# Performance work log

Measured on AMD Instinct MI355X. Metric: run time of the kernel, lower is better.

## Reference

```python
import jax, jax.numpy as jnp
import numpy as np

IN_FEATURES = 1024
OUT_FEATURES = 1024
KNOT_COUNT = 5
ORDER = 3
BATCH = 4096


def setup_inputs() -> dict:
    key = jax.random.key(0)
    k1, k2 = jax.random.split(key)
    x = jax.random.normal(k1, (BATCH, IN_FEATURES), dtype=jnp.float32)
    knots = jnp.linspace(-1.0, 1.0, KNOT_COUNT, dtype=jnp.float32)
    coeffs = jax.random.normal(k2, (KNOT_COUNT + ORDER, OUT_FEATURES, IN_FEATURES), dtype=jnp.float32)
    return {"x": x, "knots": knots, "coeffs": coeffs}


def _bspline_bases(x, knots, order):
    # x: [B, I]; knots: [K] uniform grid. Extend to K + 2*order + 1 knots so
    # the number of degree-`order` basis functions is K + order.
    h = knots[1] - knots[0]
    left = knots[0] + h * jnp.arange(-order, 0, dtype=knots.dtype)
    right = knots[-1] + h * jnp.arange(1, order + 2, dtype=knots.dtype)
    t = jnp.concatenate([left, knots, right])  # [K + 2*order + 1]
    xe = x[..., None]  # [B, I, 1]
    # degree-0 indicator bases: [B, I, m-1]
    bases = ((xe >= t[:-1]) & (xe < t[1:])).astype(x.dtype)
    # Cox-de Boor recursion up to degree `order` (vectorized over batch/features)
    for k in range(1, order + 1):
        left_num = (xe - t[: -(k + 1)]) / (t[k:-1] - t[: -(k + 1)])
        right_num = (t[k + 1:] - xe) / (t[k + 1:] - t[1:-k])
        bases = left_num * bases[..., :-1] + right_num * bases[..., 1:]
    return bases  # [B, I, K + order]


def reference(x, knots, coeffs):
    # Faithful fused version of the per-(i,j) python loops:
    # spline_j(b) = sum_n B_n(x[b,i]) * coeffs[n, j, i]; output sums over i.
    bases = _bspline_bases(x, knots, ORDER)          # [B, I, N]
    return jnp.einsum('bin,noi->bo', bases, coeffs)  # [B, O]
```

## Files before the change

### kernel.cpp

```cpp
#include <hip/hip_runtime.h>
#include <hip/hip_bf16.h>
#include <cstdint>
#include <cstddef>

#define IN_F   1024
#define OUT_F  1024
#define NB     8
#define BATCH  4096
#define KTOT   (NB * IN_F)

typedef __attribute__((ext_vector_type(4))) float  f32x4;
typedef __attribute__((ext_vector_type(8))) float  f32x8;
typedef __attribute__((ext_vector_type(8))) __bf16 bf16x8;
typedef __attribute__((ext_vector_type(4))) unsigned short u16x4;

#define GLDS16(g, l)                                                     \
    __builtin_amdgcn_global_load_lds(                                    \
        (const __attribute__((address_space(1))) void*)(g),              \
        (__attribute__((address_space(3))) void*)(l), 16, 0, 0)

__device__ __forceinline__ void spline_w(float r, float w[4]) {
    const float r2 = r * r, r3 = r2 * r;
    const float omr = 1.0f - r;
    w[0] = omr * omr * omr * (1.0f / 6.0f);
    w[1] = (3.0f * r3 - 6.0f * r2 + 4.0f) * (1.0f / 6.0f);
    w[2] = (-3.0f * r3 + 3.0f * r2 + 3.0f * r + 1.0f) * (1.0f / 6.0f);
    w[3] = r3 * (1.0f / 6.0f);
}

__global__ void k_cvt(const float* __restrict__ src, __bf16* __restrict__ dst) {
    const size_t g   = blockIdx.x * blockDim.x + threadIdx.x;
    const size_t idx = g * 8;
    const int i = (int)(idx & 1023);
    const int o = (int)((idx >> 10) & 1023);
    const int c = (i >> 3) & 7;
    const int isw = (i & ~63) | ((c ^ (o & 7)) << 3);
    f32x8 v = *(const f32x8*)(src + idx);
    bf16x8 ov = __builtin_convertvector(v, bf16x8);
    *(bf16x8*)(dst + (idx - i) + isw) = ov;
}

__global__ void k_basis(const float* __restrict__ x, __bf16* __restrict__ A) {
    const int g    = blockIdx.x * blockDim.x + threadIdx.x;
    const int flat = g * 4;
    const int b = flat >> 10, i = flat & 1023;
    f32x4 xv = *(const f32x4*)(x + flat);

    float w[4][4];
    int   jj[4];
#pragma unroll
    for (int e = 0; e < 4; ++e) {
        const float u  = (xv[e] + 2.5f) * 2.0f;
        const float jf = floorf(u);
        jj[e] = (int)jf;
        spline_w(u - jf, w[e]);
    }

    const int c   = (i >> 3) & 7;
    const int isw = (i & ~63) | ((c ^ (b & 7)) << 3) | (i & 7);
    __bf16* base = A + (size_t)b * KTOT + isw;
#pragma unroll
    for (int n = 0; n < NB; ++n) {
        u16x4 pack;
#pragma unroll
        for (int e = 0; e < 4; ++e) {
            const int d = n - jj[e] + 3;
            float v = (d == 0) ? w[e][0]
                    : (d == 1) ? w[e][1]
                    : (d == 2) ? w[e][2]
                    : (d == 3) ? w[e][3] : 0.0f;
            __bf16 h = (__bf16)v;
            pack[e] = __builtin_bit_cast(unsigned short, h);
        }
        *(u16x4*)(base + n * IN_F) = pack;
    }
}

#define BM 128
#define BN 128
#define BK 64
#define NT (KTOT / BK)
#define SPLITK 2
#define NTS (NT / SPLITK)

__global__ __launch_bounds__(512) void k_gemm(const __bf16* __restrict__ A,
                                              const __bf16* __restrict__ W,
                                              float* __restrict__ C,
                                              float* __restrict__ P) {
    __shared__ __align__(16) char ls[2][32768];

    const int tid  = threadIdx.x;
    const int o0   = blockIdx.x * BN;
    const int b0   = blockIdx.y * BM;
    const int kz   = blockIdx.z;
    const int lane = tid & 63;
    const int wv   = tid >> 6;
    const int wr   = wv >> 2;
    const int wc   = wv & 3;
    const int l15  = lane & 15;
    const int lhi  = lane >> 4;

    f32x4 acc[4][2] = {};

    const int srow  = tid >> 3;
    const int scol8 = (tid & 7) * 8;

    auto STAGE = [&](int buf, int kt) {
        const int k0 = kt * BK;
        const int n  = k0 >> 10;
        const int i0 = k0 & 1023;
        char* la = ls[buf];
        char* lb = ls[buf] + 16384;
#pragma unroll
        for (int it = 0; it < 2; ++it) {
            const __bf16* ga = A + (size_t)(b0 + srow + it * 64) * KTOT + k0 + scol8;
            GLDS16(ga, la + tid * 16 + it * 8192);
        }
#pragma unroll
        for (int it = 0; it < 2; ++it) {
            const __bf16* gw = W + ((size_t)n << 20)
                                 + (size_t)(o0 + srow + it * 64) * IN_F + i0 + scol8;
            GLDS16(gw, lb + tid * 16 + it * 8192);
        }
    };

    const int ktBeg = kz * NTS;
    STAGE(0, ktBeg);
    __syncthreads();

    int cur = 0;
    for (int kt = ktBeg; kt < ktBeg + NTS; ++kt) {
        if (kt + 1 < ktBeg + NTS) STAGE(cur ^ 1, kt + 1);
        const char* la = ls[cur];
        const char* lb = ls[cur] + 16384;
#pragma unroll
        for (int kk = 0; kk < BK; kk += 32) {
            bf16x8 af[4], bfr[2];
#pragma unroll
            for (int m = 0; m < 4; ++m) {
                const int r = wr * 64 + m * 16 + l15;
                const int c = ((kk >> 3) + lhi) ^ (r & 7);
                af[m] = *(const bf16x8*)(la + r * 128 + c * 16);
            }
#pragma unroll
            for (int nn = 0; nn < 2; ++nn) {
                const int r = wc * 32 + nn * 16 + l15;
                const int c = ((kk >> 3) + lhi) ^ (r & 7);
                bfr[nn] = *(const bf16x8*)(lb + r * 128 + c * 16);
            }
#pragma unroll
            for (int m = 0; m < 4; ++m)
#pragma unroll
                for (int nn = 0; nn < 2; ++nn)
                    acc[m][nn] = __builtin_amdgcn_mfma_f32_16x16x32_bf16(
                        af[m], bfr[nn], acc[m][nn], 0, 0, 0);
        }
        __syncthreads();
        cur ^= 1;
    }

    float* dst = (kz == 0) ? C : P;
    const int crow = lhi * 4;
#pragma unroll
    for (int m = 0; m < 4; ++m) {
#pragma unroll
        for (int nn = 0; nn < 2; ++nn) {
            float* cp = dst + (size_t)(b0 + wr * 64 + m * 16 + crow) * OUT_F
                            + o0 + wc * 32 + nn * 16 + l15;
#pragma unroll
            for (int j = 0; j < 4; ++j)
                cp[(size_t)j * OUT_F] = acc[m][nn][j];
        }
    }
}

__global__ void k_add(float* __restrict__ C, const float* __restrict__ P) {
    const size_t g = (size_t)(blockIdx.x * blockDim.x + threadIdx.x) * 4;
    f32x4 a = *(const f32x4*)(C + g);
    f32x4 b = *(const f32x4*)(P + g);
    a += b;
    *(f32x4*)(C + g) = a;
}

__global__ void k_naive(const float* __restrict__ x, const float* __restrict__ coeffs,
                        float* __restrict__ out) {
    const int b = blockIdx.y * 16 + (threadIdx.x >> 4);
    const int o = blockIdx.x * 16 + (threadIdx.x & 15);
    float sum = 0.0f;
    for (int i = 0; i < IN_F; ++i) {
        const float u  = (x[(size_t)b * IN_F + i] + 2.5f) * 2.0f;
        const float jf = floorf(u);
        const int   j  = (int)jf;
        float w[4];
        spline_w(u - jf, w);
#pragma unroll
        for (int m = 0; m < 4; ++m) {
            const int idx = j - 3 + m;
            if (idx >= 0 && idx < NB)
                sum += w[m] * coeffs[(size_t)idx * OUT_F * IN_F + (size_t)o * IN_F + i];
        }
    }
    out[(size_t)b * OUT_F + o] = sum;
}

extern "C" void kernel_launch(void* const* d_in, const int* in_sizes, int n_in,
                              void* d_out, int out_size, void* d_ws, size_t ws_size,
                              hipStream_t stream) {
    const float* x      = (const float*)d_in[0];
    const float* coeffs = (const float*)d_in[2];
    float* out = (float*)d_out;

    const size_t needA = (size_t)BATCH * KTOT * sizeof(__bf16);
    const size_t needW = (size_t)NB * OUT_F * IN_F * sizeof(__bf16);
    const size_t needP = (size_t)BATCH * OUT_F * sizeof(float);

    if (ws_size >= needA + needW + needP) {
        __bf16* A  = (__bf16*)d_ws;
        __bf16* Wb = (__bf16*)((char*)d_ws + needA);
        float*  P  = (float*)((char*)d_ws + needA + needW);

        hipLaunchKernelGGL(k_cvt, dim3(NB * OUT_F * IN_F / 8 / 256), dim3(256), 0,
                           stream, coeffs, Wb);
        hipLaunchKernelGGL(k_basis, dim3(BATCH * IN_F / 4 / 256), dim3(256), 0,
                           stream, x, A);
        hipLaunchKernelGGL(k_gemm, dim3(OUT_F / BN, BATCH / BM, SPLITK), dim3(512),
                           0, stream, A, Wb, out, P);
        hipLaunchKernelGGL(k_add, dim3(BATCH * OUT_F / 4 / 256), dim3(256), 0,
                           stream, out, P);
    } else if (ws_size >= needA + needW) {
        __bf16* A  = (__bf16*)d_ws;
        __bf16* Wb = (__bf16*)((char*)d_ws + needA);
        hipLaunchKernelGGL(k_cvt, dim3(NB * OUT_F * IN_F / 8 / 256), dim3(256), 0,
                           stream, coeffs, Wb);
        hipLaunchKernelGGL(k_basis, dim3(BATCH * IN_F / 4 / 256), dim3(256), 0,
                           stream, x, A);
        hipLaunchKernelGGL(k_naive, dim3(OUT_F / 16, BATCH / 16), dim3(256), 0,
                           stream, x, coeffs, out);
    } else {
        hipLaunchKernelGGL(k_naive, dim3(OUT_F / 16, BATCH / 16), dim3(256), 0,
                           stream, x, coeffs, out);
    }
}
```

Baseline: 132.8 us.

## Enlarge GEMM tile to 256x128, triple-buffer LDS, and remap blocks across XCDs

The bf16 GEMM tile grows from 128x128 to 256x128, so each wave now computes a 64x64 sub-tile. This gives more MFMA work per LDS fragment load and raises arithmetic intensity. Double buffering becomes a three-stage LDS pipeline that uses explicit vmcnt waits and raw barriers, so global-to-LDS loads run further ahead of compute. A flat 256-block grid is remapped so neighbouring batch tiles land on the same XCD for L2 reuse. The costs are 144KB of LDS, which limits occupancy to one block per CU, a higher accumulator register count, and dropping an unused fallback path.

```diff
diff --git a/kernel.cpp b/kernel.cpp
--- a/kernel.cpp
+++ b/kernel.cpp
@@ -76,31 +76,38 @@
     }
 }
 
-#define BM 128
+#define BM 256
 #define BN 128
 #define BK 64
 #define NT (KTOT / BK)
 #define SPLITK 2
 #define NTS (NT / SPLITK)
+#define BUFSZ 49152
 
 __global__ __launch_bounds__(512) void k_gemm(const __bf16* __restrict__ A,
                                               const __bf16* __restrict__ W,
                                               float* __restrict__ C,
                                               float* __restrict__ P) {
-    __shared__ __align__(16) char ls[2][32768];
-
+    __shared__ __align__(16) char ls[3 * BUFSZ];
+
+    const int fid = blockIdx.x;
+    const int xcd = fid & 7;
+    const int s   = fid >> 3;
+    const int y   = xcd + 8 * (s & 1);
+    const int xb  = (s >> 1) & 7;
+    const int kz  = s >> 4;
+
+    const int o0   = xb * BN;
+    const int b0   = y * BM;
     const int tid  = threadIdx.x;
-    const int o0   = blockIdx.x * BN;
-    const int b0   = blockIdx.y * BM;
-    const int kz   = blockIdx.z;
     const int lane = tid & 63;
     const int wv   = tid >> 6;
-    const int wr   = wv >> 2;
-    const int wc   = wv & 3;
+    const int wr   = wv >> 1;
+    const int wc   = wv & 1;
     const int l15  = lane & 15;
     const int lhi  = lane >> 4;
 
-    f32x4 acc[4][2] = {};
+    f32x4 acc[4][4] = {};
 
     const int srow  = tid >> 3;
     const int scol8 = (tid & 7) * 8;
@@ -109,10 +116,10 @@
         const int k0 = kt * BK;
         const int n  = k0 >> 10;
         const int i0 = k0 & 1023;
-        char* la = ls[buf];
-        char* lb = ls[buf] + 16384;
-#pragma unroll
-        for (int it = 0; it < 2; ++it) {
+        char* la = ls + buf * BUFSZ;
+        char* lb = la + 32768;
+#pragma unroll
+        for (int it = 0; it < 4; ++it) {
             const __bf16* ga = A + (size_t)(b0 + srow + it * 64) * KTOT + k0 + scol8;
             GLDS16(ga, la + tid * 16 + it * 8192);
         }
@@ -126,16 +133,22 @@
 
     const int ktBeg = kz * NTS;
     STAGE(0, ktBeg);
-    __syncthreads();
-
-    int cur = 0;
-    for (int kt = ktBeg; kt < ktBeg + NTS; ++kt) {
-        if (kt + 1 < ktBeg + NTS) STAGE(cur ^ 1, kt + 1);
-        const char* la = ls[cur];
-        const char* lb = ls[cur] + 16384;
+    STAGE(1, ktBeg + 1);
+
+    int cur = 0, nxt = 2;
+    for (int t = 0; t < NTS; ++t) {
+        if (t < NTS - 1) asm volatile("s_waitcnt vmcnt(6)" ::: "memory");
+        else             asm volatile("s_waitcnt vmcnt(0)" ::: "memory");
+        __builtin_amdgcn_s_barrier();
+        __builtin_amdgcn_sched_barrier(0);
+
+        if (t + 2 < NTS) STAGE(nxt, ktBeg + t + 2);
+
+        const char* la = ls + cur * BUFSZ;
+        const char* lb = la + 32768;
 #pragma unroll
         for (int kk = 0; kk < BK; kk += 32) {
-            bf16x8 af[4], bfr[2];
+            bf16x8 af[4], bfr[4];
 #pragma unroll
             for (int m = 0; m < 4; ++m) {
                 const int r = wr * 64 + m * 16 + l15;
@@ -143,20 +156,20 @@
                 af[m] = *(const bf16x8*)(la + r * 128 + c * 16);
             }
 #pragma unroll
-            for (int nn = 0; nn < 2; ++nn) {
-                const int r = wc * 32 + nn * 16 + l15;
+            for (int nn = 0; nn < 4; ++nn) {
+                const int r = wc * 64 + nn * 16 + l15;
                 const int c = ((kk >> 3) + lhi) ^ (r & 7);
                 bfr[nn] = *(const bf16x8*)(lb + r * 128 + c * 16);
             }
 #pragma unroll
             for (int m = 0; m < 4; ++m)
 #pragma unroll
-                for (int nn = 0; nn < 2; ++nn)
+                for (int nn = 0; nn < 4; ++nn)
                     acc[m][nn] = __builtin_amdgcn_mfma_f32_16x16x32_bf16(
                         af[m], bfr[nn], acc[m][nn], 0, 0, 0);
         }
-        __syncthreads();
-        cur ^= 1;
+        cur = (cur == 2) ? 0 : cur + 1;
+        nxt = (nxt == 2) ? 0 : nxt + 1;
     }
 
     float* dst = (kz == 0) ? C : P;
@@ -164,9 +177,9 @@
 #pragma unroll
     for (int m = 0; m < 4; ++m) {
 #pragma unroll
-        for (int nn = 0; nn < 2; ++nn) {
+        for (int nn = 0; nn < 4; ++nn) {
             float* cp = dst + (size_t)(b0 + wr * 64 + m * 16 + crow) * OUT_F
-                            + o0 + wc * 32 + nn * 16 + l15;
+                            + o0 + wc * 64 + nn * 16 + l15;
 #pragma unroll
             for (int j = 0; j < 4; ++j)
                 cp[(size_t)j * OUT_F] = acc[m][nn][j];
@@ -223,19 +236,9 @@
                            stream, coeffs, Wb);
         hipLaunchKernelGGL(k_basis, dim3(BATCH * IN_F / 4 / 256), dim3(256), 0,
                            stream, x, A);
-        hipLaunchKernelGGL(k_gemm, dim3(OUT_F / BN, BATCH / BM, SPLITK), dim3(512),
-                           0, stream, A, Wb, out, P);
+        hipLaunchKernelGGL(k_gemm, dim3(256), dim3(512), 0, stream, A, Wb, out, P);
         hipLaunchKernelGGL(k_add, dim3(BATCH * OUT_F / 4 / 256), dim3(256), 0,
                            stream, out, P);
-    } else if (ws_size >= needA + needW) {
-        __bf16* A  = (__bf16*)d_ws;
-        __bf16* Wb = (__bf16*)((char*)d_ws + needA);
-        hipLaunchKernelGGL(k_cvt, dim3(NB * OUT_F * IN_F / 8 / 256), dim3(256), 0,
-                           stream, coeffs, Wb);
-        hipLaunchKernelGGL(k_basis, dim3(BATCH * IN_F / 4 / 256), dim3(256), 0,
-                           stream, x, A);
-        hipLaunchKernelGGL(k_naive, dim3(OUT_F / 16, BATCH / 16), dim3(256), 0,
-                           stream, x, coeffs, out);
     } else {
         hipLaunchKernelGGL(k_naive, dim3(OUT_F / 16, BATCH / 16), dim3(256), 0,
                            stream, x, coeffs, out);
```

Result: faster. 121.1 us (-8.8%).
